# Kernel optimization log

Measured on AMD Instinct MI355X. Metric: run time of the kernel, lower is better.

Reference implementation:

```python
import jax, jax.numpy as jnp
import numpy as np

WIN = 2048      # window_size / conv kernel size
HOP = 128       # hop_size / conv stride
SR = 22050
N_MELS = 128
N_FREQ = WIN // 2 + 1  # 1025


def _fourier_weights(window_size=WIN):
    # Faithful to get_fourier_weights_for_mel (hanning=True)
    frec = np.linspace(-window_size // 2, 0, window_size // 2 + 1)
    time = np.linspace(0, window_size - 1, window_size)
    hann = np.hanning(window_size)
    cos_f = np.array([np.cos(2 * np.pi * f * time / window_size) for f in frec])
    sin_f = np.array([np.sin(2 * np.pi * f * time / window_size) for f in frec])
    return cos_f[::-1] * hann, sin_f[::-1] * hann


def _hz_to_mel(f):
    # librosa slaney mel scale
    f = np.atleast_1d(np.asarray(f, dtype=np.float64))
    f_sp = 200.0 / 3.0
    mels = f / f_sp
    min_log_hz = 1000.0
    min_log_mel = min_log_hz / f_sp
    logstep = np.log(6.4) / 27.0
    log_t = f >= min_log_hz
    mels[log_t] = min_log_mel + np.log(f[log_t] / min_log_hz) / logstep
    return mels


def _mel_to_hz(m):
    m = np.atleast_1d(np.asarray(m, dtype=np.float64))
    f_sp = 200.0 / 3.0
    freqs = f_sp * m
    min_log_hz = 1000.0
    min_log_mel = min_log_hz / f_sp
    logstep = np.log(6.4) / 27.0
    log_t = m >= min_log_mel
    freqs[log_t] = min_log_hz * np.exp(logstep * (m[log_t] - min_log_mel))
    return freqs


def _mel_filterbank(sr=SR, n_fft=WIN, n_mels=N_MELS, fmin=0.0, fmax=None):
    # Faithful to librosa.filters.mel (htk=False, norm='slaney')
    if fmax is None:
        fmax = sr / 2.0
    fftfreqs = np.linspace(0.0, sr / 2.0, n_fft // 2 + 1)
    mel_pts = np.linspace(_hz_to_mel(fmin)[0], _hz_to_mel(fmax)[0], n_mels + 2)
    mel_f = _mel_to_hz(mel_pts)                       # [n_mels+2]
    fdiff = np.diff(mel_f)
    ramps = mel_f[:, None] - fftfreqs[None, :]
    lower = -ramps[:-2] / fdiff[:-1, None]
    upper = ramps[2:] / fdiff[1:, None]
    weights = np.maximum(0.0, np.minimum(lower, upper))  # [n_mels, n_freq]
    enorm = 2.0 / (mel_f[2:n_mels + 2] - mel_f[:n_mels])
    return weights * enorm[:, None]


def setup_inputs() -> dict:
    key = jax.random.key(0)
    B, T = 8, 2048 + 128 * 5151  # -> n_frames = 5152
    x = jax.random.normal(key, (B, 1, T), dtype=jnp.float32)
    cos_np, sin_np = _fourier_weights()
    return {
        "x": x,
        "cos_w": jnp.asarray(np.ascontiguousarray(cos_np), dtype=jnp.float32),  # [1025, 2048]
        "sin_w": jnp.asarray(np.ascontiguousarray(sin_np), dtype=jnp.float32),  # [1025, 2048]
        "mel_w": jnp.asarray(_mel_filterbank(), dtype=jnp.float32),             # [128, 1025]
    }


def reference(x, cos_w, sin_w, mel_w):
    # x: [B, 1, T]
    T = x.shape[-1]
    n_frames = (T - WIN) // HOP + 1
    idx = jnp.arange(n_frames)[:, None] * HOP + jnp.arange(WIN)[None, :]
    frames = x[:, 0, :][:, idx]
    c = jnp.einsum('btw,fw->bft', frames, cos_w)     # [B, N_FREQ, n_frames]
    s = jnp.einsum('btw,fw->bft', frames, sin_w)
    power = c * c + s * s                            # power spectrum
    mel = jnp.einsum('mf,bft->bmt', mel_w, power)    # 1x1 conv == channel matmul
    return mel  # in_db=False default
```

## Files before the change

### kernel.cpp

```cpp
#include <hip/hip_runtime.h>
#include <stdint.h>

#define NB 8
#define TLEN 661376
#define NFR 5152
#define NFREQ 1025
#define NMEL 128
#define NFRP 5376
#define OUT_BT (NMEL * NFR)

typedef unsigned int u32;
typedef float f32x4 __attribute__((ext_vector_type(4)));
typedef short s16x8 __attribute__((ext_vector_type(8)));
typedef u32 u32x4 __attribute__((ext_vector_type(4)));

__device__ __forceinline__ u32 f2bf(float f) {
  u32 u = __float_as_uint(f);
  return (u + 0x7FFFu + ((u >> 16) & 1u)) >> 16;
}
__device__ __forceinline__ u32 packbf(float a, float b) {
  return f2bf(a) | (f2bf(b) << 16);
}
__device__ __forceinline__ void bar_lgkm() {
  asm volatile("s_waitcnt lgkmcnt(0)" ::: "memory");
  __builtin_amdgcn_s_barrier();
  __builtin_amdgcn_sched_barrier(0);
}

#define WCAN_BYTES 9437184
#define MCAN_OFF   9437184
#define MCAN_BYTES 294912
#define P_OFF      9732096
#define P_ROWB     2304
#define TIER1_NEED 108822528ULL
#define TIER2_NEED 61636608ULL
#define TIER3_NEED 42762240ULL

__global__ void prep_wcan(const float* __restrict__ cw, const float* __restrict__ sw,
                          char* __restrict__ wg) {
  int id = blockIdx.x * 256 + threadIdx.x;
  int jp = id & 3, l15 = (id >> 2) & 15, l4 = (id >> 6) & 3;
  int fr = (id >> 8) & 15, k = (id >> 12) & 63, g = id >> 18;
  if (g >= 9) return;
  int freq = g * 128 + (fr >> 1) * 16 + l15;
  const float* src = (fr & 1) ? sw : cw;
  u32 pk = 0;
  if (freq < NFREQ) {
    int smp = k * 32 + l4 * 8 + jp * 2;
    pk = packbf(src[(size_t)freq * 2048 + smp], src[(size_t)freq * 2048 + smp + 1]);
  }
  *(u32*)(wg + (size_t)id * 4) = pk;
}

__global__ void prep_mcan(const float* __restrict__ mw, char* __restrict__ mg) {
  int id = blockIdx.x * 256 + threadIdx.x;
  if (id >= 73728) return;
  int jp = id & 3, l15 = (id >> 2) & 15, l4 = (id >> 6) & 3;
  int fr = (id >> 8) & 7, ks = id >> 11;
  int m = fr * 16 + l15;
  int f = ks * 32 + l4 * 8 + jp * 2;
  float v0 = (f < NFREQ) ? mw[(size_t)m * NFREQ + f] : 0.f;
  float v1 = (f + 1 < NFREQ) ? mw[(size_t)m * NFREQ + f + 1] : 0.f;
  *(u32*)(mg + (size_t)id * 4) = packbf(v0, v1);
}

#define K1_X 69376
#define K1_LDS 118528
__global__ __launch_bounds__(512, 2) void k1_power(
    const float* __restrict__ x, const char* __restrict__ wg,
    char* __restrict__ P, int tstart, int tcap) {
  __shared__ __align__(16) char smem[K1_LDS];
  const int tid = threadIdx.x;
  const int lane = tid & 63, wid = tid >> 6;
  const int l15 = lane & 15, l4 = lane >> 4;
  const int fw = wid & 3, tw = wid >> 2;
  const int tb = blockIdx.x, g = blockIdx.y, b = blockIdx.z;
  const int t0 = tstart + tb * 256;

  {
    const float* xb = x + (size_t)b * TLEN;
    const int sbase = t0 * 128;
#pragma unroll
    for (int i = 0; i < 9; ++i) {
      int q = tid + i * 512;
      if (q < 4336) {
        int s0 = sbase + q * 8;
        u32 r0, r1, r2, r3;
        if (s0 + 8 <= TLEN) {
          f32x4 v0 = *(const f32x4*)(xb + s0);
          f32x4 v1 = *(const f32x4*)(xb + s0 + 4);
          r0 = packbf(v0[0], v0[1]); r1 = packbf(v0[2], v0[3]);
          r2 = packbf(v1[0], v1[1]); r3 = packbf(v1[2], v1[3]);
        } else {
          float e[8];
#pragma unroll
          for (int j = 0; j < 8; ++j) { int s = s0 + j; e[j] = (s < TLEN) ? xb[s] : 0.f; }
          r0 = packbf(e[0], e[1]); r1 = packbf(e[2], e[3]);
          r2 = packbf(e[4], e[5]); r3 = packbf(e[6], e[7]);
        }
        int lb = q * 16;
        *(u32x4*)(smem + (lb ^ (((lb >> 8) & 7) << 4))) = (u32x4){r0, r1, r2, r3};
      }
    }
  }

  f32x4 acc[4][8];
#pragma unroll
  for (int i = 0; i < 4; ++i)
#pragma unroll
    for (int j = 0; j < 8; ++j) acc[i][j] = (f32x4){0.f, 0.f, 0.f, 0.f};

  const char* wslab = wg + (size_t)g * (64 * 16384);
  char* ring = smem + K1_X;

  int bfbase[8], bfkey[8];
#pragma unroll
  for (int nt = 0; nt < 8; ++nt) {
    int lt = tw * 128 + nt * 16 + l15;
    bfbase[nt] = lt * 256 + l4 * 16;
    bfkey[nt] = lt & 7;
  }
  const int afoff = (fw * 4) * 1024 + l4 * 256 + l15 * 16;

  {
    u32x4 a0 = *(const u32x4*)(wslab + tid * 16);
    u32x4 a1 = *(const u32x4*)(wslab + tid * 16 + 8192);
    u32x4 b0 = *(const u32x4*)(wslab + 16384 + tid * 16);
    u32x4 b1 = *(const u32x4*)(wslab + 16384 + tid * 16 + 8192);
    *(u32x4*)(ring + tid * 16) = a0;
    *(u32x4*)(ring + tid * 16 + 8192) = a1;
    *(u32x4*)(ring + 16384 + tid * 16) = b0;
    *(u32x4*)(ring + 16384 + tid * 16 + 8192) = b1;
  }
  u32x4 wr0 = *(const u32x4*)(wslab + 2 * 16384 + tid * 16);
  u32x4 wr1 = *(const u32x4*)(wslab + 2 * 16384 + tid * 16 + 8192);
  bar_lgkm();

  s16x8 af[4], bf[8];
#pragma unroll
  for (int m4 = 0; m4 < 4; ++m4)
    af[m4] = *(const s16x8*)(ring + afoff + m4 * 1024);
#pragma unroll
  for (int nt = 0; nt < 8; ++nt)
    bf[nt] = *(const s16x8*)(smem + (bfbase[nt] ^ ((bfkey[nt] & 7) << 4)));

  int rd_n = 16384, wr_n = 32768;
  for (int k = 0; k < 64; ++k) {
    __builtin_amdgcn_s_setprio(1);
#pragma unroll
    for (int m4 = 0; m4 < 4; ++m4)
#pragma unroll
      for (int nt = 0; nt < 8; ++nt)
        acc[m4][nt] = __builtin_amdgcn_mfma_f32_16x16x32_bf16(af[m4], bf[nt],
                                                              acc[m4][nt], 0, 0, 0);
    __builtin_amdgcn_s_setprio(0);

    if (k + 1 < 64) {
      const char* rb = ring + rd_n;
#pragma unroll
      for (int m4 = 0; m4 < 4; ++m4)
        af[m4] = *(const s16x8*)(rb + afoff + m4 * 1024);
      const int kn = k + 1, kq = kn >> 2;
#pragma unroll
      for (int nt = 0; nt < 8; ++nt) {
        int a = bfbase[nt] + kn * 64;
        bf[nt] = *(const s16x8*)(smem + (a ^ (((bfkey[nt] + kq) & 7) << 4)));
      }
    }
    if (k + 2 < 64) {
      char* wb = ring + wr_n;
      *(u32x4*)(wb + tid * 16) = wr0;
      *(u32x4*)(wb + tid * 16 + 8192) = wr1;
    }
    if (k + 3 < 64) {
      const char* ns = wslab + (k + 3) * 16384;
      wr0 = *(const u32x4*)(ns + tid * 16);
      wr1 = *(const u32x4*)(ns + tid * 16 + 8192);
    }
    rd_n += 16384; if (rd_n == 49152) rd_n = 0;
    wr_n += 16384; if (wr_n == 49152) wr_n = 0;
    bar_lgkm();
  }

  char* plds = smem + K1_X;
#pragma unroll
  for (int h = 0; h < 2; ++h) {
    if (tw == h) {
#pragma unroll
      for (int q = 0; q < 2; ++q)
#pragma unroll
        for (int nt = 0; nt < 8; ++nt) {
          f32x4 c = acc[q * 2][nt], s = acc[q * 2 + 1][nt];
          float p0 = c[0] * c[0] + s[0] * s[0];
          float p1 = c[1] * c[1] + s[1] * s[1];
          float p2 = c[2] * c[2] + s[2] * s[2];
          float p3 = c[3] * c[3] + s[3] * s[3];
          int lt = nt * 16 + l15;
          int fl = fw * 32 + q * 16 + l4 * 4;
          int a = lt * 256 + fl * 2;
          int sw = (lt & 7) << 4;
          *(u32*)(plds + (a ^ sw)) = packbf(p0, p1);
          *(u32*)(plds + ((a + 4) ^ sw)) = packbf(p2, p3);
        }
    }
    bar_lgkm();
#pragma unroll
    for (int i = 0; i < 4; ++i) {
      int lin = (tid + i * 512) * 16;
      u32x4 v = *(const u32x4*)(plds + (lin ^ (((lin >> 8) & 7) << 4)));
      int tc = tb * 256 + h * 128 + (lin >> 8);
      *(u32x4*)(P + ((size_t)b * tcap + tc) * P_ROWB + g * 256 + (lin & 255)) = v;
    }
    bar_lgkm();
  }
}

__global__ __launch_bounds__(256, 4) void k2_mel(
    const char* __restrict__ P, const char* __restrict__ mg,
    float* __restrict__ out, int tstart, int tcap) {
  __shared__ __align__(16) char sm[4096];
  const int tid = threadIdx.x;
  const int lane = tid & 63, wid = tid >> 6;
  const int l15 = lane & 15, l4 = lane >> 4;
  const int tb = blockIdx.x, b = blockIdx.y;
  const int tz = tb * 64;

  const int st_t = tid >> 2, st_fo = tid & 3;
  const char* prow = P + ((size_t)b * tcap + tz + st_t) * P_ROWB + st_fo * 16;

  f32x4 acc[2][4];
#pragma unroll
  for (int i = 0; i < 2; ++i)
#pragma unroll
    for (int j = 0; j < 4; ++j) acc[i][j] = (f32x4){0.f, 0.f, 0.f, 0.f};

  u32x4 pr = *(const u32x4*)prow;
  const int lw = (st_t * 64 + st_fo * 16) ^ ((st_t & 7) << 4);
  const int afo = l4 * 256 + l15 * 16;

  for (int ks = 0; ks < 36; ++ks) {
    *(u32x4*)(sm + lw) = pr;
    bar_lgkm();
    if (ks + 1 < 36) pr = *(const u32x4*)(prow + (ks + 1) * 64);
    s16x8 a0 = *(const s16x8*)(mg + (size_t)(ks * 8 + wid * 2) * 1024 + afo);
    s16x8 a1 = *(const s16x8*)(mg + (size_t)(ks * 8 + wid * 2 + 1) * 1024 + afo);
    s16x8 bf[4];
#pragma unroll
    for (int nt = 0; nt < 4; ++nt) {
      int a = ((nt * 16 + l15) * 64 + l4 * 16) ^ ((l15 & 7) << 4);
      bf[nt] = *(const s16x8*)(sm + a);
    }
#pragma unroll
    for (int nt = 0; nt < 4; ++nt) {
      acc[0][nt] = __builtin_amdgcn_mfma_f32_16x16x32_bf16(a0, bf[nt], acc[0][nt], 0, 0, 0);
      acc[1][nt] = __builtin_amdgcn_mfma_f32_16x16x32_bf16(a1, bf[nt], acc[1][nt], 0, 0, 0);
    }
    bar_lgkm();
  }

#pragma unroll
  for (int nt = 0; nt < 4; ++nt) {
    int t = tstart + tz + nt * 16 + l15;
    if (t < NFR) {
#pragma unroll
      for (int mf = 0; mf < 2; ++mf)
#pragma unroll
        for (int ii = 0; ii < 4; ++ii) {
          int m = wid * 32 + mf * 16 + l4 * 4 + ii;
          out[(size_t)b * OUT_BT + (size_t)m * NFR + t] = acc[mf][nt][ii];
        }
    }
  }
}

#define F_BT 96
#define F_NTT 54
#define F_NGRP 17
#define F_GI_TOT 1088
#define F_SLABB 8192
#define F_XSB 28416
#define F_XS_OFF 0
#define F_WL_OFF 28416
#define F_PL_OFF 36608
#define F_ML_OFF 48896
#define F_LDS_TOT 65280
#define F_WS_MG 8912896
#define F_WS_NEED 9191424
#define F_MLB 16384

__device__ __forceinline__ int f_swzW(int a) { return a ^ (((a >> 6) & 7) << 4); }
__device__ __forceinline__ int f_swzR(int a) { return a ^ (((a >> 7) & 7) << 4); }

__global__ void f_prep_w(const float* __restrict__ cw, const float* __restrict__ sw,
                         char* __restrict__ wg) {
  int id = blockIdx.x * 256 + threadIdx.x;
  int j = id & 15, r = (id >> 4) & 127, gi = id >> 11;
  if (gi >= F_GI_TOT) return;
  int g = gi >> 6, k0 = gi & 63;
  int c = r >> 5, r5 = r & 31;
  int f = g * 64 + c * 16 + (r5 & 15);
  const float* src = (r5 < 16) ? cw : sw;
  u32 pk = 0;
  if (f < NFREQ) {
    int k = k0 * 32 + j * 2;
    pk = packbf(src[(size_t)f * 2048 + k], src[(size_t)f * 2048 + k + 1]);
  }
  *(u32*)(wg + (size_t)gi * F_SLABB + r * 64 + j * 4) = pk;
}

__global__ void f_prep_mel(const float* __restrict__ mw, char* __restrict__ mg) {
  int id = blockIdx.x * 256 + threadIdx.x;
  int fp = id & 31, m = (id >> 5) & 127, g = id >> 12;
  if (g >= F_NGRP) return;
  int f = g * 64 + fp * 2;
  float v0 = (f < NFREQ) ? mw[m * NFREQ + f] : 0.f;
  float v1 = (f + 1 < NFREQ) ? mw[m * NFREQ + f + 1] : 0.f;
  int a = m * 128 + fp * 4;
  *(u32*)(mg + (size_t)g * F_MLB + (a ^ ((m & 7) << 4))) = packbf(v0, v1);
}

template <bool PRIM>
__global__ __launch_bounds__(512, 4) void f_mel_main(
    const float* __restrict__ x, const char* __restrict__ wg,
    const char* __restrict__ mg, const float* __restrict__ cw,
    const float* __restrict__ sw, const float* __restrict__ mw,
    float* __restrict__ out) {
  __shared__ __align__(16) char smem[F_LDS_TOT];
  const int tid = threadIdx.x;
  const int lane = tid & 63, wid = tid >> 6;
  const int l15 = lane & 15, l4 = lane >> 4;
  const int bid = blockIdx.x;
  const int b = bid / F_NTT, tt = bid - b * F_NTT;
  const int t0 = tt * F_BT;
  const int c2 = wid >> 1, jh = wid & 1;

  {
    const float* xb = x + (size_t)b * TLEN + (size_t)t0 * 128;
    const int qn = (TLEN - t0 * 128) >> 3;
    for (int it = 0; it < 4; ++it) {
      int q = tid + it * 512;
      if (q < F_XSB / 16) {
        u32 r0 = 0, r1 = 0, r2 = 0, r3 = 0;
        if (q < qn) {
          f32x4 v0 = *(const f32x4*)(xb + q * 8);
          f32x4 v1 = *(const f32x4*)(xb + q * 8 + 4);
          r0 = packbf(v0[0], v0[1]); r1 = packbf(v0[2], v0[3]);
          r2 = packbf(v1[0], v1[1]); r3 = packbf(v1[2], v1[3]);
        }
        int a = q * 16;
        int ph = a ^ ((((a >> 8) + t0) & 7) << 4);
        *(u32x4*)(smem + F_XS_OFF + ph) = (u32x4){r0, r1, r2, r3};
      }
    }
  }

  f32x4 acc[2][3];
  f32x4 mel[6];
#pragma unroll
  for (int i = 0; i < 2; ++i)
#pragma unroll
    for (int j = 0; j < 3; ++j) acc[i][j] = (f32x4){0.f, 0.f, 0.f, 0.f};
#pragma unroll
  for (int i = 0; i < 6; ++i) mel[i] = (f32x4){0.f, 0.f, 0.f, 0.f};

  u32x4 wr_p = {0, 0, 0, 0};
  f32x4 wf0 = {0, 0, 0, 0}, wf1 = {0, 0, 0, 0};
  const int wr_r = tid >> 2, wr_j = tid & 3;
  const int wr_c = wr_r >> 5, wr_r5 = wr_r & 31;

  auto loadW = [&](int gi) {
    if (PRIM) {
      wr_p = *(const u32x4*)(wg + (size_t)gi * F_SLABB + tid * 16);
    } else {
      int g = gi >> 6, k0 = gi & 63;
      int f = g * 64 + wr_c * 16 + (wr_r5 & 15);
      if (f < NFREQ) {
        const float* src = (wr_r5 < 16) ? cw : sw;
        const float* p = src + (size_t)f * 2048 + k0 * 32 + wr_j * 8;
        wf0 = *(const f32x4*)p;
        wf1 = *(const f32x4*)(p + 4);
      } else {
        wf0 = (f32x4){0, 0, 0, 0};
        wf1 = (f32x4){0, 0, 0, 0};
      }
    }
  };

  loadW(0);

  for (int gi = 0; gi < F_GI_TOT; ++gi) {
    const int g = gi >> 6, k0 = gi & 63;
    {
      int a = tid * 16;
      u32x4 v;
      if (PRIM) v = wr_p;
      else v = (u32x4){packbf(wf0[0], wf0[1]), packbf(wf0[2], wf0[3]),
                       packbf(wf1[0], wf1[1]), packbf(wf1[2], wf1[3])};
      *(u32x4*)(smem + F_WL_OFF + f_swzW(a)) = v;
    }
    if (k0 == 0) {
      for (int i = 0; i < 2; ++i) {
        int h = tid + i * 512;
        if (PRIM) {
          u32x4 v = *(const u32x4*)(mg + (size_t)g * F_MLB + h * 16);
          *(u32x4*)(smem + F_ML_OFF + h * 16) = v;
        } else {
          int m = h >> 3, part = h & 7;
          int f0 = g * 64 + part * 8;
          u32 w[4];
#pragma unroll
          for (int e = 0; e < 4; ++e) {
            int f = f0 + e * 2;
            float v0 = (f < NFREQ) ? mw[m * NFREQ + f] : 0.f;
            float v1 = (f + 1 < NFREQ) ? mw[m * NFREQ + f + 1] : 0.f;
            w[e] = packbf(v0, v1);
          }
          int a = m * 128 + part * 16;
          *(u32x4*)(smem + F_ML_OFF + (a ^ ((m & 7) << 4))) = (u32x4){w[0], w[1], w[2], w[3]};
        }
      }
    }
    __syncthreads();
    if (gi + 1 < F_GI_TOT) loadW(gi + 1);

    const int kb = l4 * 16;
    s16x8 bf[3], af[2];
    const int xkey = (k0 >> 2) + t0;
#pragma unroll
    for (int nt = 0; nt < 3; ++nt) {
      const int lt = jh * 48 + nt * 16 + l15;
      const int lb = lt * 256 + k0 * 64 + kb;
      bf[nt] = *(const s16x8*)(smem + F_XS_OFF + (lb ^ (((lt + xkey) & 7) << 4)));
    }
#pragma unroll
    for (int cs = 0; cs < 2; ++cs) {
      const int row = c2 * 32 + cs * 16 + l15;
      af[cs] = *(const s16x8*)(smem + F_WL_OFF + f_swzW(row * 64 + kb));
    }
#pragma unroll
    for (int cs = 0; cs < 2; ++cs)
#pragma unroll
      for (int nt = 0; nt < 3; ++nt)
        acc[cs][nt] = __builtin_amdgcn_mfma_f32_16x16x32_bf16(af[cs], bf[nt],
                                                              acc[cs][nt], 0, 0, 0);

    if (k0 == 63) {
#pragma unroll
      for (int nt = 0; nt < 3; ++nt) {
        f32x4 pc = acc[0][nt], ps = acc[1][nt];
        float p0 = pc[0] * pc[0] + ps[0] * ps[0];
        float p1 = pc[1] * pc[1] + ps[1] * ps[1];
        float p2 = pc[2] * pc[2] + ps[2] * ps[2];
        float p3 = pc[3] * pc[3] + ps[3] * ps[3];
        const int t = jh * 48 + nt * 16 + l15;
        const int a0 = t * 128 + c2 * 32 + l4 * 8;
        const int sw = (t & 7) << 4;
        *(u32*)(smem + F_PL_OFF + (a0 ^ sw)) = packbf(p0, p1);
        *(u32*)(smem + F_PL_OFF + ((a0 + 4) ^ sw)) = packbf(p2, p3);
      }
#pragma unroll
      for (int i = 0; i < 2; ++i)
#pragma unroll
        for (int j = 0; j < 3; ++j) acc[i][j] = (f32x4){0.f, 0.f, 0.f, 0.f};
      __syncthreads();

      const int mrow = wid * 16 + l15;
#pragma unroll
      for (int ks = 0; ks < 2; ++ks) {
        s16x8 a2 = *(const s16x8*)(smem + F_ML_OFF + f_swzR(mrow * 128 + ks * 64 + kb));
#pragma unroll
        for (int n2 = 0; n2 < 6; ++n2) {
          const int tr = n2 * 16 + l15;
          s16x8 b2 = *(const s16x8*)(smem + F_PL_OFF + f_swzR(tr * 128 + ks * 64 + kb));
          mel[n2] = __builtin_amdgcn_mfma_f32_16x16x32_bf16(a2, b2, mel[n2], 0, 0, 0);
        }
      }
    }
    __syncthreads();
  }

#pragma unroll
  for (int n2 = 0; n2 < 6; ++n2) {
    const int t = t0 + n2 * 16 + l15;
    if (t < NFR) {
#pragma unroll
      for (int ii = 0; ii < 4; ++ii) {
        const int m = wid * 16 + l4 * 4 + ii;
        out[(size_t)b * OUT_BT + (size_t)m * NFR + t] = mel[n2][ii];
      }
    }
  }
}

extern "C" void kernel_launch(void* const* d_in, const int* in_sizes, int n_in,
                              void* d_out, int out_size, void* d_ws, size_t ws_size,
                              hipStream_t stream) {
  if (n_in < 4) return;
  const float* x  = (const float*)d_in[0];
  const float* cw = (const float*)d_in[1];
  const float* sw = (const float*)d_in[2];
  const float* mw = (const float*)d_in[3];
  float* out = (float*)d_out;
  char* ws = (char*)d_ws;

  int nchunks = 0, tcap = 0;
  int cstart[3], ctb[3];
  if (d_ws && ws_size >= TIER1_NEED) {
    nchunks = 1; tcap = 5376;
    cstart[0] = 0; ctb[0] = 21;
  } else if (d_ws && ws_size >= TIER2_NEED) {
    nchunks = 2; tcap = 2816;
    cstart[0] = 0; ctb[0] = 11; cstart[1] = 2816; ctb[1] = 10;
  } else if (d_ws && ws_size >= TIER3_NEED) {
    nchunks = 3; tcap = 1792;
    cstart[0] = 0; ctb[0] = 7; cstart[1] = 1792; ctb[1] = 7;
    cstart[2] = 3584; ctb[2] = 7;
  }

  if (nchunks > 0) {
    char* wg = ws;
    char* mg = ws + MCAN_OFF;
    char* P  = ws + P_OFF;
    prep_wcan<<<9216, 256, 0, stream>>>(cw, sw, wg);
    prep_mcan<<<288, 256, 0, stream>>>(mw, mg);
    for (int c = 0; c < nchunks; ++c) {
      dim3 g1(ctb[c], 9, NB);
      k1_power<<<g1, 512, 0, stream>>>(x, wg, P, cstart[c], tcap);
      dim3 g2(ctb[c] * 4, NB);
      k2_mel<<<g2, 256, 0, stream>>>(P, mg, out, cstart[c], tcap);
    }
    return;
  }

  const bool prim = (d_ws != nullptr) && (ws_size >= (size_t)F_WS_NEED);
  if (prim) {
    f_prep_w<<<F_GI_TOT * 2048 / 256, 256, 0, stream>>>(cw, sw, ws);
    f_prep_mel<<<F_NGRP * 4096 / 256, 256, 0, stream>>>(mw, ws + F_WS_MG);
    f_mel_main<true><<<NB * F_NTT, 512, 0, stream>>>(x, ws, ws + F_WS_MG,
                                                     cw, sw, mw, out);
  } else {
    f_mel_main<false><<<NB * F_NTT, 512, 0, stream>>>(x, nullptr, nullptr,
                                                      cw, sw, mw, out);
  }
}
```

Baseline: 440.2 us.

## Interleave LDS fragment loads and weight staging with MFMA groups in main loop

Restructures the main MFMA K-loop so the 32 MFMAs per step are split into four groups. Each group is followed by the next step's B-fragment and A-fragment LDS reads plus one slice of the global-to-LDS weight staging, all fenced by sched_barrier. A-fragments and staging registers are double-buffered and the loop is unrolled by two so buffers swap without copies. Swizzle address math is simplified to one base and key. The aim is to hide LDS and global latency behind matrix ops, at the cost of extra registers for the second A-fragment and staging buffers.

```diff
diff --git a/kernel.cpp b/kernel.cpp
--- a/kernel.cpp
+++ b/kernel.cpp
@@ -113,14 +113,8 @@
   const char* wslab = wg + (size_t)g * (64 * 16384);
   char* ring = smem + K1_X;
 
-  int bfbase[8], bfkey[8];
-#pragma unroll
-  for (int nt = 0; nt < 8; ++nt) {
-    int lt = tw * 128 + nt * 16 + l15;
-    bfbase[nt] = lt * 256 + l4 * 16;
-    bfkey[nt] = lt & 7;
-  }
-  const int afoff = (fw * 4) * 1024 + l4 * 256 + l15 * 16;
+  const int bfb = (tw * 128 + l15) * 256 + l4 * 16;
+  const int afoff = fw * 4096 + l4 * 256 + l15 * 16;
 
   {
     u32x4 a0 = *(const u32x4*)(wslab + tid * 16);
@@ -132,54 +126,62 @@
     *(u32x4*)(ring + 16384 + tid * 16) = b0;
     *(u32x4*)(ring + 16384 + tid * 16 + 8192) = b1;
   }
-  u32x4 wr0 = *(const u32x4*)(wslab + 2 * 16384 + tid * 16);
-  u32x4 wr1 = *(const u32x4*)(wslab + 2 * 16384 + tid * 16 + 8192);
+  u32x4 wrA0 = *(const u32x4*)(wslab + 2 * 16384 + tid * 16);
+  u32x4 wrA1 = *(const u32x4*)(wslab + 2 * 16384 + tid * 16 + 8192);
+  u32x4 wrB0 = {0, 0, 0, 0}, wrB1 = {0, 0, 0, 0};
   bar_lgkm();
 
-  s16x8 af[4], bf[8];
-#pragma unroll
-  for (int m4 = 0; m4 < 4; ++m4)
-    af[m4] = *(const s16x8*)(ring + afoff + m4 * 1024);
-#pragma unroll
-  for (int nt = 0; nt < 8; ++nt)
-    bf[nt] = *(const s16x8*)(smem + (bfbase[nt] ^ ((bfkey[nt] & 7) << 4)));
-
-  int rd_n = 16384, wr_n = 32768;
-  for (int k = 0; k < 64; ++k) {
-    __builtin_amdgcn_s_setprio(1);
-#pragma unroll
-    for (int m4 = 0; m4 < 4; ++m4)
-#pragma unroll
-      for (int nt = 0; nt < 8; ++nt)
-        acc[m4][nt] = __builtin_amdgcn_mfma_f32_16x16x32_bf16(af[m4], bf[nt],
-                                                              acc[m4][nt], 0, 0, 0);
-    __builtin_amdgcn_s_setprio(0);
-
-    if (k + 1 < 64) {
-      const char* rb = ring + rd_n;
-#pragma unroll
-      for (int m4 = 0; m4 < 4; ++m4)
-        af[m4] = *(const s16x8*)(rb + afoff + m4 * 1024);
-      const int kn = k + 1, kq = kn >> 2;
-#pragma unroll
-      for (int nt = 0; nt < 8; ++nt) {
-        int a = bfbase[nt] + kn * 64;
-        bf[nt] = *(const s16x8*)(smem + (a ^ (((bfkey[nt] + kq) & 7) << 4)));
-      }
-    }
-    if (k + 2 < 64) {
-      char* wb = ring + wr_n;
-      *(u32x4*)(wb + tid * 16) = wr0;
-      *(u32x4*)(wb + tid * 16 + 8192) = wr1;
-    }
-    if (k + 3 < 64) {
-      const char* ns = wslab + (k + 3) * 16384;
-      wr0 = *(const u32x4*)(ns + tid * 16);
-      wr1 = *(const u32x4*)(ns + tid * 16 + 8192);
-    }
-    rd_n += 16384; if (rd_n == 49152) rd_n = 0;
-    wr_n += 16384; if (wr_n == 49152) wr_n = 0;
-    bar_lgkm();
+  s16x8 afA[4], afB[4], bf[8];
+  {
+    const int key0 = (l15 & 7) << 4;
+#pragma unroll
+    for (int q = 0; q < 4; ++q)
+      afA[q] = *(const s16x8*)(ring + afoff + q * 1024);
+#pragma unroll
+    for (int nt = 0; nt < 8; ++nt)
+      bf[nt] = *(const s16x8*)(smem + ((bfb + nt * 4096) ^ key0));
+  }
+  bar_lgkm();
+
+  auto iter = [&](int k, s16x8 (&afc)[4], s16x8 (&afn)[4],
+                  u32x4& wc0, u32x4& wc1, u32x4& wn0, u32x4& wn1) {
+    const char* rnext = ring + ((k + 1) % 3) * 16384;
+    char* rwr = ring + ((k + 2) % 3) * 16384;
+    const int kn = k + 1;
+    const int key = ((l15 + (kn >> 2)) & 7) << 4;
+    const int ab = bfb + kn * 64;
+#pragma unroll
+    for (int q = 0; q < 4; ++q) {
+      __builtin_amdgcn_s_setprio(1);
+#pragma unroll
+      for (int m4 = 0; m4 < 4; ++m4) {
+        acc[m4][2 * q] = __builtin_amdgcn_mfma_f32_16x16x32_bf16(
+            afc[m4], bf[2 * q], acc[m4][2 * q], 0, 0, 0);
+        acc[m4][2 * q + 1] = __builtin_amdgcn_mfma_f32_16x16x32_bf16(
+            afc[m4], bf[2 * q + 1], acc[m4][2 * q + 1], 0, 0, 0);
+      }
+      __builtin_amdgcn_s_setprio(0);
+      if (kn < 64) {
+        bf[2 * q] = *(const s16x8*)(smem + ((ab + (2 * q) * 4096) ^ key));
+        bf[2 * q + 1] = *(const s16x8*)(smem + ((ab + (2 * q + 1) * 4096) ^ key));
+        afn[q] = *(const s16x8*)(rnext + afoff + q * 1024);
+      }
+      if (q == 0 && k + 2 < 64) *(u32x4*)(rwr + tid * 16) = wc0;
+      if (q == 1 && k + 2 < 64) *(u32x4*)(rwr + tid * 16 + 8192) = wc1;
+      if (q == 2 && k + 3 < 64)
+        wn0 = *(const u32x4*)(wslab + (size_t)(k + 3) * 16384 + tid * 16);
+      if (q == 3 && k + 3 < 64)
+        wn1 = *(const u32x4*)(wslab + (size_t)(k + 3) * 16384 + tid * 16 + 8192);
+      __builtin_amdgcn_sched_barrier(0);
+    }
+    asm volatile("s_waitcnt lgkmcnt(0)" ::: "memory");
+    __builtin_amdgcn_s_barrier();
+    __builtin_amdgcn_sched_barrier(0);
+  };
+
+  for (int kk = 0; kk < 32; ++kk) {
+    iter(2 * kk, afA, afB, wrA0, wrA1, wrB0, wrB1);
+    iter(2 * kk + 1, afB, afA, wrB0, wrB1, wrA0, wrA1);
   }
 
   char* plds = smem + K1_X;
```

After: 411.8 us. 1.07x faster.
